# Optimization experiments

Hardware: AMD Instinct MI355X
Metric: run time of the kernel (lower is better)

The kernel has to match this reference:

```python
import jax, jax.numpy as jnp
import numpy as np

B, L, S, D_MODEL, H = 4, 2048, 2048, 512, 8
E = D_MODEL // H  # head dim = 64


def setup_inputs() -> dict:
    key = jax.random.key(0)
    ks = jax.random.split(key, 11)
    s = 1.0 / np.sqrt(D_MODEL)
    return {
        "queries": jax.random.normal(ks[0], (B, L, D_MODEL), jnp.float32),
        "keys": jax.random.normal(ks[1], (B, S, D_MODEL), jnp.float32),
        "values": jax.random.normal(ks[2], (B, S, D_MODEL), jnp.float32),
        "Wq": jax.random.normal(ks[3], (D_MODEL, D_MODEL), jnp.float32) * s,
        "bq": jnp.zeros((D_MODEL,), jnp.float32),
        "Wk": jax.random.normal(ks[4], (D_MODEL, D_MODEL), jnp.float32) * s,
        "bk": jnp.zeros((D_MODEL,), jnp.float32),
        "Wv": jax.random.normal(ks[5], (D_MODEL, D_MODEL), jnp.float32) * s,
        "bv": jnp.zeros((D_MODEL,), jnp.float32),
        "Wo": jax.random.normal(ks[6], (D_MODEL, D_MODEL), jnp.float32) * s,
        "bo": jnp.zeros((D_MODEL,), jnp.float32),
    }


def reference(queries, keys, values, Wq, bq, Wk, bk, Wv, bv, Wo, bo):
    # QKV projections, then split heads: [B, T, H, E]
    q = (queries @ Wq + bq).reshape(B, L, H, E)
    k = (keys @ Wk + bk).reshape(B, S, H, E)
    v = (values @ Wv + bv).reshape(B, S, H, E)
    scale = 1.0 / np.sqrt(E)
    # Naive full attention: materialized [B, H, L, S] scores (as in original)
    scores = jnp.einsum('blhe,bshe->bhls', q, k)
    A = jax.nn.softmax(scale * scores, axis=-1)  # dropout = identity at eval
    out = jnp.einsum('bhls,bshd->blhd', A, v).reshape(B, L, H * E)
    return out @ Wo + bo
```

## Files before the change

kernel.cpp:

```cpp
#include <hip/hip_runtime.h>
#include <hip/hip_bf16.h>


typedef __attribute__((ext_vector_type(8))) short bf8_t;
typedef __attribute__((ext_vector_type(4))) float f4_t;
typedef __attribute__((ext_vector_type(16))) float f16_t;
typedef __attribute__((ext_vector_type(4))) unsigned int u32x4;

#define D_MODEL 512
#define HEADS 8
#define EDIM 64
#define LSEQ 2048
#define NBATCH 4
#define MTOT (NBATCH * LSEQ)
#define N4 (MTOT * D_MODEL / 4)

static __device__ __forceinline__ unsigned short f2bf(float f) {
  union { float f; unsigned int u; } x;
  x.f = f;
  unsigned int u = x.u;
  u += 0x7FFFu + ((u >> 16) & 1u);
  return (unsigned short)(u >> 16);
}

static __device__ __forceinline__ unsigned int pack2bf(float a, float b) {
  union { __hip_bfloat162 h; unsigned int u; } c;
  c.h.x = __float2bfloat16(a);
  c.h.y = __float2bfloat16(b);
  return c.u;
}

#define GLOAD_LDS(gptr, lptr)                                                        \
  __builtin_amdgcn_global_load_lds((const __attribute__((address_space(1))) void*)(gptr), \
                                   (__attribute__((address_space(3))) void*)(lptr), 16, 0, 0)

__global__ void prep_all(const float* __restrict__ q, const float* __restrict__ k,
                         const float* __restrict__ v,
                         const float* __restrict__ Wq, const float* __restrict__ Wk,
                         const float* __restrict__ Wv, const float* __restrict__ Wo,
                         unsigned short* __restrict__ Xq, unsigned short* __restrict__ Xk,
                         unsigned short* __restrict__ Xv,
                         unsigned short* __restrict__ Wqt, unsigned short* __restrict__ Wkt,
                         unsigned short* __restrict__ Wvt, unsigned short* __restrict__ Wot) {
  __shared__ float tile[64][65];
  const int blk = blockIdx.x;
  if (blk < 12288) {
    int i = blk * 256 + threadIdx.x;
    int which = i >> 20;
    int idx = i & (N4 - 1);
    const float* in = (which == 0) ? q : (which == 1) ? k : v;
    unsigned short* out = (which == 0) ? Xq : (which == 1) ? Xk : Xv;
    float4 x = ((const float4*)in)[idx];
    ushort4 o;
    o.x = f2bf(x.x); o.y = f2bf(x.y); o.z = f2bf(x.z); o.w = f2bf(x.w);
    ((ushort4*)out)[idx] = o;
  } else {
    const int b = blk - 12288;
    const int which = b >> 6;
    const int b2 = b & 63;
    const int k0 = (b2 >> 3) * 64, n0 = (b2 & 7) * 64;
    const float* W = (which == 0) ? Wq : (which == 1) ? Wk : (which == 2) ? Wv : Wo;
    unsigned short* Wt = (which == 0) ? Wqt : (which == 1) ? Wkt : (which == 2) ? Wvt : Wot;
    const int tx = threadIdx.x & 63;
    const int ty = threadIdx.x >> 6;
#pragma unroll
    for (int i = 0; i < 64; i += 4)
      tile[i + ty][tx] = W[(size_t)(k0 + i + ty) * D_MODEL + n0 + tx];
    __syncthreads();
#pragma unroll
    for (int i = 0; i < 64; i += 4)
      Wt[(size_t)(n0 + i + ty) * D_MODEL + k0 + tx] = f2bf(tile[tx][i + ty]);
  }
}

__device__ __forceinline__ void stage_a(const unsigned short* __restrict__ A,
                                        unsigned short* lA, int m0, int k0) {
  const int t = threadIdx.x;
  int rowA = t >> 2, cbA = (t & 3) * 16;
  GLOAD_LDS((const char*)(A + (size_t)(m0 + rowA) * D_MODEL + k0) + cbA, (char*)lA + t * 16);
}
__device__ __forceinline__ void stage_b(const unsigned short* __restrict__ Bt,
                                        unsigned short* lB, int n0, int k0) {
  const int t = threadIdx.x;
#pragma unroll
  for (int ii = 0; ii < 2; ++ii) {
    int c = t + ii * 256;
    int rowB = c >> 2, cbB = (c & 3) * 16;
    GLOAD_LDS((const char*)(Bt + (size_t)(n0 + rowB) * D_MODEL + k0) + cbB, (char*)lB + c * 16);
  }
}

__device__ __forceinline__ void gemm_core(const unsigned short* __restrict__ A,
                                          const unsigned short* __restrict__ Bt,
                                          unsigned short* __restrict__ lAv,
                                          unsigned short* __restrict__ lBv,
                                          f4_t (&acc)[2][4], int m0, int n0) {
  const int t = threadIdx.x;
  const int lane = t & 63;
  const int w = t >> 6;
  const int wr = w >> 1, wc = w & 1;
  const int r = lane & 15, g = lane >> 4;
  const int ASZ = 64 * 32, BSZ = 128 * 32;

  stage_a(A, lAv, m0, 0);
  stage_b(Bt, lBv, n0, 0);
  __syncthreads();

  int cur = 0;
  const int NK = D_MODEL / 32;
  for (int ks = 0; ks < NK; ++ks) {
    if (ks + 1 < NK) {
      const int kn = (ks + 1) * 32;
      stage_a(A, lAv + (cur ^ 1) * ASZ, m0, kn);
      stage_b(Bt, lBv + (cur ^ 1) * BSZ, n0, kn);
    }

    bf8_t af[2], bfv[4];
    const unsigned short* lA = lAv + cur * ASZ;
#pragma unroll
    for (int mi = 0; mi < 2; ++mi)
      af[mi] = *(const bf8_t*)(lA + (wr * 32 + mi * 16 + r) * 32 + g * 8);
    const unsigned short* lB = lBv + cur * BSZ;
#pragma unroll
    for (int ni = 0; ni < 4; ++ni)
      bfv[ni] = *(const bf8_t*)(lB + (wc * 64 + ni * 16 + r) * 32 + g * 8);
#pragma unroll
    for (int mi = 0; mi < 2; ++mi)
#pragma unroll
      for (int ni = 0; ni < 4; ++ni)
        acc[mi][ni] = __builtin_amdgcn_mfma_f32_16x16x32_bf16(af[mi], bfv[ni], acc[mi][ni], 0, 0, 0);
    __syncthreads();
    cur ^= 1;
  }
}

#define QSCALE 0.18033688011112042f
__global__ __launch_bounds__(256, 6) void qkv_gemm(
    const unsigned short* __restrict__ Xq, const unsigned short* __restrict__ Xk,
    const unsigned short* __restrict__ Xv,
    const unsigned short* __restrict__ Wqt, const unsigned short* __restrict__ Wkt,
    const unsigned short* __restrict__ Wvt,
    const float* __restrict__ bq, const float* __restrict__ bk, const float* __restrict__ bv,
    unsigned short* __restrict__ Qh, unsigned short* __restrict__ Kh,
    unsigned short* __restrict__ Vt) {
  __shared__ alignas(16) unsigned short lA[2][64 * 32];
  __shared__ alignas(16) unsigned short lB[2][128 * 32];
  const int p = blockIdx.x;
  const int res = p & 7, q = p >> 3;
  const int xx = q & 3;
  const int grp = res + ((q >> 2) << 3);
  const int z = grp >> 7;
  const int y = grp & 127;
  const int n0 = xx * 128, m0 = y * 64;

  const unsigned short* A  = (z == 0) ? Xq : (z == 1) ? Xk : Xv;
  const unsigned short* Bt = (z == 0) ? Wqt : (z == 1) ? Wkt : Wvt;
  const float* bias        = (z == 0) ? bq : (z == 1) ? bk : bv;

  f4_t acc[2][4] = {};
  gemm_core(A, Bt, &lA[0][0], &lB[0][0], acc, m0, n0);

  const int lane = threadIdx.x & 63;
  const int w = threadIdx.x >> 6;
  const int wr = w >> 1, wc = w & 1;
  const int r = lane & 15, g = lane >> 4;
#pragma unroll
  for (int mi = 0; mi < 2; ++mi)
#pragma unroll
    for (int ni = 0; ni < 4; ++ni) {
      const int coln = n0 + wc * 64 + ni * 16 + r;
      const float bv_ = bias[coln];
      const int h = coln >> 6, e = coln & 63;
#pragma unroll
      for (int j = 0; j < 4; ++j) {
        const int rowm = m0 + wr * 32 + mi * 16 + g * 4 + j;
        const int b = rowm >> 11, li = rowm & 2047;
        float v = acc[mi][ni][j] + bv_;
        if (z == 0) {
          v *= QSCALE;
          Qh[(((size_t)(b * HEADS + h) * LSEQ + li) << 6) + e] = f2bf(v);
        } else if (z == 1) {
          Kh[(((size_t)(b * HEADS + h) * LSEQ + li) << 6) + e] = f2bf(v);
        } else {
          const int bb = (li >> 2) & 3;
          const int bs = ((bb & 1) << 1) | (bb >> 1);
          const int lp = (li & ~15) | (bs << 2) | (li & 3);
          Vt[(((size_t)(b * HEADS + h) * EDIM + e) << 11) + lp] = f2bf(v);
        }
      }
    }
}

__global__ __launch_bounds__(256, 6) void o_gemm(const unsigned short* __restrict__ A,
                                                 const unsigned short* __restrict__ Bt,
                                                 const float* __restrict__ bias,
                                                 float* __restrict__ Cout) {
  __shared__ alignas(16) unsigned short lA[2][64 * 32];
  __shared__ alignas(16) unsigned short lB[2][128 * 32];
  const int p = blockIdx.x;
  const int res = p & 7, q = p >> 3;
  const int xx = q & 3;
  const int grp = res + ((q >> 2) << 3);
  const int n0 = xx * 128, m0 = grp * 64;

  f4_t acc[2][4] = {};
  gemm_core(A, Bt, &lA[0][0], &lB[0][0], acc, m0, n0);

  const int lane = threadIdx.x & 63;
  const int w = threadIdx.x >> 6;
  const int wr = w >> 1, wc = w & 1;
  const int r = lane & 15, g = lane >> 4;
#pragma unroll
  for (int mi = 0; mi < 2; ++mi)
#pragma unroll
    for (int ni = 0; ni < 4; ++ni) {
      const int coln = n0 + wc * 64 + ni * 16 + r;
      const float bv_ = bias[coln];
#pragma unroll
      for (int j = 0; j < 4; ++j) {
        const int rowm = m0 + wr * 32 + mi * 16 + g * 4 + j;
        Cout[(size_t)rowm * D_MODEL + coln] = acc[mi][ni][j] + bv_;
      }
    }
}

#define XSTR 68

__device__ __forceinline__ void stage_K1(const unsigned short* __restrict__ Kbase,
                                         unsigned short* ldsK, int s0, int tg) {
  int row = tg >> 3, col = tg & 7;
  int colp = col ^ (row & 7);
  GLOAD_LDS((const char*)(Kbase + (size_t)(s0 + row) * EDIM + colp * 8),
            (char*)ldsK + tg * 16);
}
__device__ __forceinline__ void stage_V1(const unsigned short* __restrict__ Vbase,
                                         unsigned short* ldsV, int s0, int tg) {
  int row = tg >> 3, col = tg & 7;
  int colp = col ^ (row & 7);
  GLOAD_LDS((const char*)(Vbase + (size_t)row * LSEQ + s0 + colp * 8),
            (char*)ldsV + tg * 16);
}

__global__ __launch_bounds__(1024, 4) void flash_attn(const unsigned short* __restrict__ Qh,
                                                      const unsigned short* __restrict__ Kh,
                                                      const unsigned short* __restrict__ Vt,
                                                      unsigned short* __restrict__ Ao) {
  __shared__ alignas(16) unsigned short stg[2][3][2][64 * 64];

  const int t = threadIdx.x;
  const int lane = t & 63;
  const int w = t >> 6;
  const int wg = w >> 3;
  const int wq = w & 7;
  const int tg = t & 511;
  const int qn = lane & 31;
  const int hi = lane >> 5;
  const int p = blockIdx.x;
  const int xcd = p & 7, jj = p >> 3;
  const int bh = xcd * 4 + (jj >> 3);
  const int qblk = jj & 7;
  const int q0 = qblk * 256 + wq * 32;
  const int sbase = wg * (LSEQ / 2);

  bf8_t qf[4];
#pragma unroll
  for (int kst = 0; kst < 4; ++kst)
    qf[kst] = *(const bf8_t*)(Qh + ((size_t)bh * LSEQ + q0 + qn) * EDIM + kst * 16 + hi * 8);

  float l_lane = 0.f;
  f16_t oacc[2];
#pragma unroll
  for (int eh = 0; eh < 2; ++eh)
#pragma unroll
    for (int r = 0; r < 16; ++r) oacc[eh][r] = 0.f;

  f16_t kZero;
#pragma unroll
  for (int r = 0; r < 16; ++r) kZero[r] = 0.f;

  const unsigned short* Kbase = Kh + (size_t)bh * LSEQ * EDIM;
  const unsigned short* Vbase = Vt + (size_t)bh * EDIM * LSEQ;

  unsigned short *rK = &stg[wg][0][0][0], *rV = &stg[wg][0][1][0];
  unsigned short *nK = &stg[wg][1][0][0], *nV = &stg[wg][1][1][0];
  unsigned short *sK = &stg[wg][2][0][0], *sV = &stg[wg][2][1][0];

  stage_K1(Kbase, rK, sbase, tg);
  stage_V1(Vbase, rV, sbase, tg);
  stage_K1(Kbase, nK, sbase + 64, tg);
  stage_V1(Vbase, nV, sbase + 64, tg);
  asm volatile("s_waitcnt vmcnt(2)" ::: "memory");
  __builtin_amdgcn_s_barrier();
  __builtin_amdgcn_sched_barrier(0);

  const int NT = LSEQ / 2 / 64;
  for (int kt = 0; kt < NT; ++kt) {
    if (kt + 2 < NT) {
      stage_K1(Kbase, sK, sbase + (kt + 2) * 64, tg);
      stage_V1(Vbase, sV, sbase + (kt + 2) * 64, tg);
    }
    const unsigned short* lsK = rK;
    const unsigned short* lsV = rV;

    bf8_t kf[2][4];
#pragma unroll
    for (int sh = 0; sh < 2; ++sh)
#pragma unroll
      for (int kst = 0; kst < 4; ++kst) {
        const int row = 32 * sh + qn;
        const int ch = (2 * kst + hi) ^ (row & 7);
        kf[sh][kst] = *(const bf8_t*)(&lsK[row * 64 + ch * 8]);
      }
    f16_t sacc[2];
#pragma unroll
    for (int sh = 0; sh < 2; ++sh) {
      sacc[sh] = __builtin_amdgcn_mfma_f32_32x32x16_bf16(kf[sh][0], qf[0], kZero, 0, 0, 0);
#pragma unroll
      for (int kst = 1; kst < 4; ++kst)
        sacc[sh] = __builtin_amdgcn_mfma_f32_32x32x16_bf16(kf[sh][kst], qf[kst], sacc[sh], 0, 0, 0);
    }

    unsigned int pk[16];
#pragma unroll
    for (int sh = 0; sh < 2; ++sh)
#pragma unroll
      for (int i = 0; i < 8; ++i) {
        const float a = __builtin_amdgcn_exp2f(sacc[sh][2 * i]);
        const float b = __builtin_amdgcn_exp2f(sacc[sh][2 * i + 1]);
        l_lane += a + b;
        pk[sh * 8 + i] = pack2bf(a, b);
      }

    bf8_t pvb[4];
#pragma unroll
    for (int t2 = 0; t2 < 4; ++t2) {
      union { u32x4 u; bf8_t b; } pb;
      pb.u[0] = pk[4 * t2 + 0];
      pb.u[1] = pk[4 * t2 + 1];
      pb.u[2] = pk[4 * t2 + 2];
      pb.u[3] = pk[4 * t2 + 3];
      pvb[t2] = pb.b;
    }

#pragma unroll
    for (int eh = 0; eh < 2; ++eh)
#pragma unroll
      for (int t2 = 0; t2 < 4; ++t2) {
        const int row = 32 * eh + qn;
        const int ch = (2 * t2 + hi) ^ (row & 7);
        const bf8_t vf = *(const bf8_t*)(&lsV[row * 64 + ch * 8]);
        oacc[eh] = __builtin_amdgcn_mfma_f32_32x32x16_bf16(vf, pvb[t2], oacc[eh], 0, 0, 0);
      }

    if (kt + 2 < NT) {
      asm volatile("s_waitcnt vmcnt(2) lgkmcnt(0)" ::: "memory");
    } else if (kt + 1 < NT) {
      asm volatile("s_waitcnt vmcnt(0) lgkmcnt(0)" ::: "memory");
    } else {
      asm volatile("s_waitcnt lgkmcnt(0)" ::: "memory");
    }
    __builtin_amdgcn_s_barrier();
    __builtin_amdgcn_sched_barrier(0);

    unsigned short* tK = rK; unsigned short* tV = rV;
    rK = nK; rV = nV;
    nK = sK; nV = sV;
    sK = tK; sV = tV;
  }

  __syncthreads();

  const float l_own = l_lane + __shfl_xor(l_lane, 32);
  float* xO = (float*)&stg[0][0][0][0];
  float* xL = xO + 256 * XSTR;

  if (wg == 1) {
#pragma unroll
    for (int eh = 0; eh < 2; ++eh)
#pragma unroll
      for (int k = 0; k < 4; ++k) {
        float4 v4;
        v4.x = oacc[eh][4 * k + 0]; v4.y = oacc[eh][4 * k + 1];
        v4.z = oacc[eh][4 * k + 2]; v4.w = oacc[eh][4 * k + 3];
        *(float4*)(xO + (wq * 32 + qn) * XSTR + 32 * eh + 8 * k + 4 * hi) = v4;
      }
    if (hi == 0) xL[wq * 32 + qn] = l_own;
  }
  __syncthreads();

  if (wg == 0) {
    const float inv = 1.f / (l_own + xL[wq * 32 + qn]);
    const int b = bh >> 3, h = bh & 7;
#pragma unroll
    for (int eh = 0; eh < 2; ++eh)
#pragma unroll
      for (int k = 0; k < 4; ++k) {
        const float4 v4 = *(const float4*)(xO + (wq * 32 + qn) * XSTR + 32 * eh + 8 * k + 4 * hi);
        ushort4 ov;
        ov.x = f2bf((oacc[eh][4 * k + 0] + v4.x) * inv);
        ov.y = f2bf((oacc[eh][4 * k + 1] + v4.y) * inv);
        ov.z = f2bf((oacc[eh][4 * k + 2] + v4.z) * inv);
        ov.w = f2bf((oacc[eh][4 * k + 3] + v4.w) * inv);
        const int e = 32 * eh + 8 * k + 4 * hi;
        *(ushort4*)(Ao + ((size_t)(b * LSEQ + q0 + qn)) * D_MODEL + h * EDIM + e) = ov;
      }
  }
}

extern "C" void kernel_launch(void* const* d_in, const int* in_sizes, int n_in,
                              void* d_out, int out_size, void* d_ws, size_t ws_size,
                              hipStream_t stream) {
  const float* queries = (const float*)d_in[0];
  const float* keys    = (const float*)d_in[1];
  const float* values  = (const float*)d_in[2];
  const float* Wq = (const float*)d_in[3];
  const float* bq = (const float*)d_in[4];
  const float* Wk = (const float*)d_in[5];
  const float* bk = (const float*)d_in[6];
  const float* Wv = (const float*)d_in[7];
  const float* bv = (const float*)d_in[8];
  const float* Wo = (const float*)d_in[9];
  const float* bo = (const float*)d_in[10];

  char* ws = (char*)d_ws;
  const size_t XSZ = (size_t)MTOT * D_MODEL * 2;
  unsigned short* Xq  = (unsigned short*)(ws + 0 * XSZ);
  unsigned short* Xk  = (unsigned short*)(ws + 1 * XSZ);
  unsigned short* Xv  = (unsigned short*)(ws + 2 * XSZ);
  unsigned short* Qh  = (unsigned short*)(ws + 3 * XSZ);
  unsigned short* Kh  = (unsigned short*)(ws + 4 * XSZ);
  unsigned short* Vt  = (unsigned short*)(ws + 5 * XSZ);
  unsigned short* Ao  = (unsigned short*)(ws + 6 * XSZ);
  unsigned short* Wqt = (unsigned short*)(ws + 7 * XSZ);
  unsigned short* Wkt = Wqt + 512 * 512;
  unsigned short* Wvt = Wkt + 512 * 512;
  unsigned short* Wot = Wvt + 512 * 512;

  prep_all<<<12544, 256, 0, stream>>>(queries, keys, values, Wq, Wk, Wv, Wo,
                                      Xq, Xk, Xv, Wqt, Wkt, Wvt, Wot);

  qkv_gemm<<<1536, 256, 0, stream>>>(
      Xq, Xk, Xv, Wqt, Wkt, Wvt, bq, bk, bv, Qh, Kh, Vt);

  flash_attn<<<256, 1024, 0, stream>>>(Qh, Kh, Vt, Ao);

  o_gemm<<<512, 256, 0, stream>>>(Ao, Wot, bo, (float*)d_out);
}
```

Before: 101.1 us.

## Software-pipeline QK^T one tile ahead and deepen K/V staging to four buffers

The attention loop now computes the QK^T scores for tile kt+1 while doing the exp/pack and PV MMAs for tile kt, ping-ponging two score register sets. The LDS staging grows from three to four K/V buffers, so global loads are issued three tiles ahead. The aim is to overlap the softmax VALU work with matrix-core work and to hide more load latency. The cost is more LDS (128KB per block) and more registers for the second score set, which could reduce occupancy or cause spills.

```diff
diff --git a/kernel.cpp b/kernel.cpp
--- a/kernel.cpp
+++ b/kernel.cpp
@@ -225,6 +225,7 @@
 }
 
 #define XSTR 68
+#define FA_NT 16
 
 __device__ __forceinline__ void stage_K1(const unsigned short* __restrict__ Kbase,
                                          unsigned short* ldsK, int s0, int tg) {
@@ -241,11 +242,84 @@
             (char*)ldsV + tg * 16);
 }
 
+__device__ __forceinline__ void fa_body(
+    const int kt, const unsigned short* __restrict__ Kbase,
+    const unsigned short* __restrict__ Vbase, const int sbase, const int tg,
+    const int qn, const int hi, const bf8_t (&qf)[4], const f16_t& kZero,
+    f16_t (&sc)[2], f16_t (&sn)[2],
+    const unsigned short* rV, const unsigned short* aK,
+    unsigned short* cK, unsigned short* cV,
+    float& l_lane, f16_t (&oacc)[2]) {
+  if (kt + 3 < FA_NT) {
+    stage_K1(Kbase, cK, sbase + (kt + 3) * 64, tg);
+    stage_V1(Vbase, cV, sbase + (kt + 3) * 64, tg);
+  }
+
+  if (kt + 1 < FA_NT) {
+    bf8_t kf2[2][4];
+#pragma unroll
+    for (int sh = 0; sh < 2; ++sh)
+#pragma unroll
+      for (int kst = 0; kst < 4; ++kst) {
+        const int row = 32 * sh + qn;
+        const int ch = (2 * kst + hi) ^ (row & 7);
+        kf2[sh][kst] = *(const bf8_t*)(&aK[row * 64 + ch * 8]);
+      }
+#pragma unroll
+    for (int sh = 0; sh < 2; ++sh) {
+      sn[sh] = __builtin_amdgcn_mfma_f32_32x32x16_bf16(kf2[sh][0], qf[0], kZero, 0, 0, 0);
+#pragma unroll
+      for (int kst = 1; kst < 4; ++kst)
+        sn[sh] = __builtin_amdgcn_mfma_f32_32x32x16_bf16(kf2[sh][kst], qf[kst], sn[sh], 0, 0, 0);
+    }
+  }
+
+  unsigned int pk[16];
+#pragma unroll
+  for (int sh = 0; sh < 2; ++sh)
+#pragma unroll
+    for (int i = 0; i < 8; ++i) {
+      const float a_ = __builtin_amdgcn_exp2f(sc[sh][2 * i]);
+      const float b_ = __builtin_amdgcn_exp2f(sc[sh][2 * i + 1]);
+      l_lane += a_ + b_;
+      pk[sh * 8 + i] = pack2bf(a_, b_);
+    }
+
+  bf8_t pvb[4];
+#pragma unroll
+  for (int t2 = 0; t2 < 4; ++t2) {
+    union { u32x4 u; bf8_t b; } pb;
+    pb.u[0] = pk[4 * t2 + 0];
+    pb.u[1] = pk[4 * t2 + 1];
+    pb.u[2] = pk[4 * t2 + 2];
+    pb.u[3] = pk[4 * t2 + 3];
+    pvb[t2] = pb.b;
+  }
+
+#pragma unroll
+  for (int eh = 0; eh < 2; ++eh)
+#pragma unroll
+    for (int t2 = 0; t2 < 4; ++t2) {
+      const int row = 32 * eh + qn;
+      const int ch = (2 * t2 + hi) ^ (row & 7);
+      const bf8_t vf = *(const bf8_t*)(&rV[row * 64 + ch * 8]);
+      oacc[eh] = __builtin_amdgcn_mfma_f32_32x32x16_bf16(vf, pvb[t2], oacc[eh], 0, 0, 0);
+    }
+
+  if (kt + 3 < FA_NT) {
+    asm volatile("s_waitcnt vmcnt(2) lgkmcnt(0)" ::: "memory");
+  } else {
+    asm volatile("s_waitcnt vmcnt(0) lgkmcnt(0)" ::: "memory");
+  }
+  __builtin_amdgcn_s_barrier();
+  __builtin_amdgcn_sched_barrier(0);
+}
+
 __global__ __launch_bounds__(1024, 4) void flash_attn(const unsigned short* __restrict__ Qh,
                                                       const unsigned short* __restrict__ Kh,
                                                       const unsigned short* __restrict__ Vt,
                                                       unsigned short* __restrict__ Ao) {
-  __shared__ alignas(16) unsigned short stg[2][3][2][64 * 64];
+  __shared__ alignas(16) unsigned short stg[2][4][2][64 * 64];
 
   const int t = threadIdx.x;
   const int lane = t & 63;
@@ -282,91 +356,53 @@
   const unsigned short* Vbase = Vt + (size_t)bh * EDIM * LSEQ;
 
   unsigned short *rK = &stg[wg][0][0][0], *rV = &stg[wg][0][1][0];
-  unsigned short *nK = &stg[wg][1][0][0], *nV = &stg[wg][1][1][0];
-  unsigned short *sK = &stg[wg][2][0][0], *sV = &stg[wg][2][1][0];
+  unsigned short *aK = &stg[wg][1][0][0], *aV = &stg[wg][1][1][0];
+  unsigned short *bK = &stg[wg][2][0][0], *bV = &stg[wg][2][1][0];
+  unsigned short *cK = &stg[wg][3][0][0], *cV = &stg[wg][3][1][0];
 
   stage_K1(Kbase, rK, sbase, tg);
   stage_V1(Vbase, rV, sbase, tg);
-  stage_K1(Kbase, nK, sbase + 64, tg);
-  stage_V1(Vbase, nV, sbase + 64, tg);
+  stage_K1(Kbase, aK, sbase + 64, tg);
+  stage_V1(Vbase, aV, sbase + 64, tg);
+  stage_K1(Kbase, bK, sbase + 128, tg);
+  stage_V1(Vbase, bV, sbase + 128, tg);
   asm volatile("s_waitcnt vmcnt(2)" ::: "memory");
   __builtin_amdgcn_s_barrier();
   __builtin_amdgcn_sched_barrier(0);
 
-  const int NT = LSEQ / 2 / 64;
-  for (int kt = 0; kt < NT; ++kt) {
-    if (kt + 2 < NT) {
-      stage_K1(Kbase, sK, sbase + (kt + 2) * 64, tg);
-      stage_V1(Vbase, sV, sbase + (kt + 2) * 64, tg);
-    }
-    const unsigned short* lsK = rK;
-    const unsigned short* lsV = rV;
-
-    bf8_t kf[2][4];
+  f16_t sA[2], sB[2];
+  {
+    bf8_t kf0[2][4];
 #pragma unroll
     for (int sh = 0; sh < 2; ++sh)
 #pragma unroll
       for (int kst = 0; kst < 4; ++kst) {
         const int row = 32 * sh + qn;
         const int ch = (2 * kst + hi) ^ (row & 7);
-        kf[sh][kst] = *(const bf8_t*)(&lsK[row * 64 + ch * 8]);
-      }
-    f16_t sacc[2];
+        kf0[sh][kst] = *(const bf8_t*)(&rK[row * 64 + ch * 8]);
+      }
 #pragma unroll
     for (int sh = 0; sh < 2; ++sh) {
-      sacc[sh] = __builtin_amdgcn_mfma_f32_32x32x16_bf16(kf[sh][0], qf[0], kZero, 0, 0, 0);
+      sA[sh] = __builtin_amdgcn_mfma_f32_32x32x16_bf16(kf0[sh][0], qf[0], kZero, 0, 0, 0);
 #pragma unroll
       for (int kst = 1; kst < 4; ++kst)
-        sacc[sh] = __builtin_amdgcn_mfma_f32_32x32x16_bf16(kf[sh][kst], qf[kst], sacc[sh], 0, 0, 0);
-    }
-
-    unsigned int pk[16];
-#pragma unroll
-    for (int sh = 0; sh < 2; ++sh)
-#pragma unroll
-      for (int i = 0; i < 8; ++i) {
-        const float a = __builtin_amdgcn_exp2f(sacc[sh][2 * i]);
-        const float b = __builtin_amdgcn_exp2f(sacc[sh][2 * i + 1]);
-        l_lane += a + b;
-        pk[sh * 8 + i] = pack2bf(a, b);
-      }
-
-    bf8_t pvb[4];
-#pragma unroll
-    for (int t2 = 0; t2 < 4; ++t2) {
-      union { u32x4 u; bf8_t b; } pb;
-      pb.u[0] = pk[4 * t2 + 0];
-      pb.u[1] = pk[4 * t2 + 1];
-      pb.u[2] = pk[4 * t2 + 2];
-      pb.u[3] = pk[4 * t2 + 3];
-      pvb[t2] = pb.b;
-    }
-
-#pragma unroll
-    for (int eh = 0; eh < 2; ++eh)
-#pragma unroll
-      for (int t2 = 0; t2 < 4; ++t2) {
-        const int row = 32 * eh + qn;
-        const int ch = (2 * t2 + hi) ^ (row & 7);
-        const bf8_t vf = *(const bf8_t*)(&lsV[row * 64 + ch * 8]);
-        oacc[eh] = __builtin_amdgcn_mfma_f32_32x32x16_bf16(vf, pvb[t2], oacc[eh], 0, 0, 0);
-      }
-
-    if (kt + 2 < NT) {
-      asm volatile("s_waitcnt vmcnt(2) lgkmcnt(0)" ::: "memory");
-    } else if (kt + 1 < NT) {
-      asm volatile("s_waitcnt vmcnt(0) lgkmcnt(0)" ::: "memory");
-    } else {
-      asm volatile("s_waitcnt lgkmcnt(0)" ::: "memory");
-    }
-    __builtin_amdgcn_s_barrier();
-    __builtin_amdgcn_sched_barrier(0);
-
-    unsigned short* tK = rK; unsigned short* tV = rV;
-    rK = nK; rV = nV;
-    nK = sK; nV = sV;
-    sK = tK; sV = tV;
-  }
+        sA[sh] = __builtin_amdgcn_mfma_f32_32x32x16_bf16(kf0[sh][kst], qf[kst], sA[sh], 0, 0, 0);
+    }
+  }
+
+#define FA_ROTATE()                                                       \
+  { unsigned short *tK_ = rK, *tV_ = rV;                                  \
+    rK = aK; rV = aV; aK = bK; aV = bV; bK = cK; bV = cV; cK = tK_; cV = tV_; }
+
+  for (int kt = 0; kt < FA_NT; kt += 2) {
+    fa_body(kt, Kbase, Vbase, sbase, tg, qn, hi, qf, kZero,
+            sA, sB, rV, aK, cK, cV, l_lane, oacc);
+    FA_ROTATE();
+    fa_body(kt + 1, Kbase, Vbase, sbase, tg, qn, hi, qf, kZero,
+            sB, sA, rV, aK, cK, cV, l_lane, oacc);
+    FA_ROTATE();
+  }
+#undef FA_ROTATE
 
   __syncthreads();
 
```

Measured after the change: 217.2 us. 115% more time.
